# Optimization experiments

Hardware: AMD Instinct MI355X
Metric: run time of the kernel (lower is better)

## Reference

```python
import jax, jax.numpy as jnp
import numpy as np


def setup_inputs() -> dict:
    key = jax.random.key(0)
    ks = jax.random.split(key, 8)
    N, E = 10000, 160000
    IN, OUT, TC = 512, 512, 256
    x = jax.random.normal(ks[0], (N, IN), dtype=jnp.float32)
    t_emb = jax.random.normal(ks[1], (TC,), dtype=jnp.float32)
    edge_index = jax.random.randint(ks[2], (2, E), 0, N, dtype=jnp.int64)
    # GCNConv weight (glorot-ish scale) and bias
    W = jax.random.normal(ks[3], (IN, OUT), dtype=jnp.float32) / np.sqrt(IN)
    b = jnp.zeros((OUT,), dtype=jnp.float32)
    # time_proj Linear(TC, OUT)
    Wt = jax.random.normal(ks[4], (TC, OUT), dtype=jnp.float32) / np.sqrt(TC)
    bt = jnp.zeros((OUT,), dtype=jnp.float32)
    return {"x": x, "t_emb": t_emb, "edge_index": edge_index,
            "W": W, "b": b, "Wt": Wt, "bt": bt}


def _gcn_conv(x, edge_index, W, b):
    # PyG GCNConv: add self-loops, symmetric normalization, xW, scatter-add, +bias
    N = x.shape[0]
    loops = jnp.arange(N, dtype=edge_index.dtype)
    src = jnp.concatenate([edge_index[0], loops])  # [E+N]
    dst = jnp.concatenate([edge_index[1], loops])
    deg = jax.ops.segment_sum(jnp.ones_like(dst, dtype=x.dtype), dst,
                              num_segments=N)  # in-degree incl. self-loop
    dinv = jnp.where(deg > 0, jax.lax.rsqrt(deg), 0.0)
    norm = dinv[src] * dinv[dst]  # [E+N]
    xw = x @ W  # [N, OUT] - transform before gather (fewer FLOPs on edges)
    msgs = norm[:, None] * xw[src]  # [E+N, OUT]
    out = jax.ops.segment_sum(msgs, dst, num_segments=N)
    return out + b


def reference(x, t_emb, edge_index, W, b, Wt, bt):
    h = _gcn_conv(x, edge_index, W, b)          # [N, OUT]
    time_emb = t_emb @ Wt + bt                   # [OUT] (1-D t_emb branch)
    return h + time_emb
```

## Files before the change

### kernel.cpp

```cpp
#include <hip/hip_runtime.h>

#define OUTC 512
#define INC 512
#define NTILE 4
#define TCOL 128
#define LDA 72
#define TPB 256
#define CAP 96

typedef __bf16 bf16x8 __attribute__((ext_vector_type(8)));
typedef float f32x4 __attribute__((ext_vector_type(4)));

static __device__ __forceinline__ unsigned short f2bf(float f) {
    unsigned u = __float_as_uint(f);
    unsigned r = u + 0x7fffu + ((u >> 16) & 1u);
    return (unsigned short)(r >> 16);
}
static __device__ __forceinline__ float bflo(unsigned r) { return __uint_as_float(r << 16); }
static __device__ __forceinline__ float bfhi(unsigned r) { return __uint_as_float(r & 0xffff0000u); }
static __device__ __forceinline__ void acc8s(float* a, uint4 v, float n) {
    a[0] += n * bflo(v.x); a[1] += n * bfhi(v.x);
    a[2] += n * bflo(v.y); a[3] += n * bfhi(v.y);
    a[4] += n * bflo(v.z); a[5] += n * bfhi(v.z);
    a[6] += n * bflo(v.w); a[7] += n * bfhi(v.w);
}

__global__ __launch_bounds__(256) void k_prep(const float* __restrict__ x,
                                              const float* __restrict__ W,
                                              const float* __restrict__ t_emb,
                                              const float* __restrict__ Wt,
                                              const float* __restrict__ bt,
                                              const float* __restrict__ b,
                                              int* __restrict__ counts,
                                              unsigned short* __restrict__ xb,
                                              unsigned short* __restrict__ wtb,
                                              float* __restrict__ temb,
                                              int ZB, int XBB,
                                              int M, int Mpad, int TC) {
    __shared__ float smem[32 * 33];
    int bid = blockIdx.x;
    if (bid < ZB) {
        int i = bid * 256 + threadIdx.x;
        if (i < M) counts[i] = 0;
    } else if (bid < ZB + XBB) {
        int idx = (bid - ZB) * 256 + threadIdx.x;
        int row = idx >> 6;
        int kg = (idx & 63) * 8;
        ushort4 h0 = make_ushort4(0, 0, 0, 0), h1 = make_ushort4(0, 0, 0, 0);
        if (row < M) {
            float4 v0 = *(const float4*)(x + (size_t)row * INC + kg);
            float4 v1 = *(const float4*)(x + (size_t)row * INC + kg + 4);
            h0 = make_ushort4(f2bf(v0.x), f2bf(v0.y), f2bf(v0.z), f2bf(v0.w));
            h1 = make_ushort4(f2bf(v1.x), f2bf(v1.y), f2bf(v1.z), f2bf(v1.w));
        }
        *(ushort4*)(xb + (size_t)row * INC + kg) = h0;
        *(ushort4*)(xb + (size_t)row * INC + kg + 4) = h1;
    } else if (bid < ZB + XBB + 256) {
        int b2 = bid - (ZB + XBB);
        int bk = (b2 & 15) * 32, bn = (b2 >> 4) * 32;
        int tx = threadIdx.x & 31, ty = threadIdx.x >> 5;
        for (int r = ty; r < 32; r += 8)
            smem[r * 33 + tx] = W[(size_t)(bk + r) * OUTC + bn + tx];
        __syncthreads();
        for (int r = ty; r < 32; r += 8)
            wtb[(size_t)(bn + r) * INC + bk + tx] = f2bf(smem[tx * 33 + r]);
    } else {
        int j = bid - (ZB + XBB + 256);
        int t = threadIdx.x;
        float p = 0.0f;
        for (int k = t; k < TC; k += 256) p += t_emb[k] * Wt[(size_t)k * OUTC + j];
        smem[t] = p;
        __syncthreads();
        for (int s = 128; s > 0; s >>= 1) {
            if (t < s) smem[t] += smem[t + s];
            __syncthreads();
        }
        if (t == 0) temb[j] = smem[0] + bt[j] + b[j];
    }
}

__global__ __launch_bounds__(256) void k_ag(const unsigned short* __restrict__ xb,
                                            const unsigned short* __restrict__ wtb,
                                            unsigned short* __restrict__ xwb,
                                            const int* __restrict__ src,
                                            const int* __restrict__ dst,
                                            int* __restrict__ counts,
                                            int* __restrict__ slots,
                                            int E, int Mpad) {
    __shared__ unsigned short la[128 * LDA];
    __shared__ unsigned short lb[128 * LDA];

    const int bid = blockIdx.x;
    const int tid = threadIdx.x;
    const int GB = (Mpad / 128) * (OUTC / 128);

    if (bid >= GB) {
        int e = (bid - GB) * 256 + tid;
        if (e < E) {
            int s = src[e];
            int d = dst[e];
            int pos = atomicAdd(&counts[d], 1);
            if (pos < CAP) slots[(size_t)d * CAP + pos] = s;
        }
        return;
    }

    const int n0 = (bid & 3) * 128;
    const int m0 = (bid >> 2) * 128;
    const int lane = tid & 63;
    const int wave = tid >> 6;
    const int wr = (wave >> 1) * 64;
    const int wc = (wave & 1) * 64;
    const int l15 = lane & 15;
    const int k8 = (lane >> 4) * 8;

    f32x4 acc[4][4];
#pragma unroll
    for (int m = 0; m < 4; ++m)
#pragma unroll
        for (int n = 0; n < 4; ++n)
            acc[m][n] = (f32x4){0.f, 0.f, 0.f, 0.f};

    for (int k0 = 0; k0 < INC; k0 += 64) {
#pragma unroll
        for (int i = 0; i < 4; ++i) {
            int f = i * 256 + tid;
            int row = f >> 3, c = f & 7;
            uint4 va = *(const uint4*)(xb + (size_t)(m0 + row) * INC + k0 + c * 8);
            *(uint4*)(&la[row * LDA + c * 8]) = va;
            uint4 vb = *(const uint4*)(wtb + (size_t)(n0 + row) * INC + k0 + c * 8);
            *(uint4*)(&lb[row * LDA + c * 8]) = vb;
        }
        __syncthreads();

#pragma unroll
        for (int kc = 0; kc < 64; kc += 32) {
            bf16x8 af[4], bf[4];
#pragma unroll
            for (int m = 0; m < 4; ++m)
                af[m] = *(const bf16x8*)(&la[(wr + m * 16 + l15) * LDA + kc + k8]);
#pragma unroll
            for (int n = 0; n < 4; ++n)
                bf[n] = *(const bf16x8*)(&lb[(wc + n * 16 + l15) * LDA + kc + k8]);
#pragma unroll
            for (int m = 0; m < 4; ++m)
#pragma unroll
                for (int n = 0; n < 4; ++n)
                    acc[m][n] = __builtin_amdgcn_mfma_f32_16x16x32_bf16(af[m], bf[n], acc[m][n], 0, 0, 0);
        }
        __syncthreads();
    }

    const int rbase = (lane >> 4) * 4;
#pragma unroll
    for (int m = 0; m < 4; ++m)
#pragma unroll
        for (int n = 0; n < 4; ++n) {
            int gcol = n0 + wc + n * 16 + l15;
            unsigned short* p = xwb + (size_t)(gcol >> 7) * Mpad * TCOL + (gcol & 127);
#pragma unroll
            for (int r = 0; r < 4; ++r) {
                int grow = m0 + wr + m * 16 + rbase + r;
                p[(size_t)grow * TCOL] = f2bf(acc[m][n][r]);
            }
        }
}

__global__ __launch_bounds__(256) void k_gather(const int* __restrict__ slots,
                                                const int* __restrict__ counts,
                                                const unsigned short* __restrict__ xwb,
                                                const float* __restrict__ temb,
                                                float* __restrict__ out, int N, int Mpad) {
    const int bid = blockIdx.x;
    const int tile = (bid & 7) >> 1;
    const int node = (bid >> 3) * 8 + (bid & 1) * 4 + (threadIdx.x >> 6);
    if (node >= N) return;
    const int lane = threadIdx.x & 63;
    const int slot = lane >> 4;
    const int c8 = (lane & 15) * 8;
    const unsigned short* basep = xwb + (size_t)tile * Mpad * TCOL + c8;

    float a[8] = {0.f, 0.f, 0.f, 0.f, 0.f, 0.f, 0.f, 0.f};
    const int deg = counts[node];
    const int dc = deg < CAP ? deg : CAP;
    const int* sp = slots + (size_t)node * CAP;
    int i = 0;
    for (; i + 8 <= dc; i += 8) {
        int sA = sp[i + slot];
        int sB = sp[i + 4 + slot];
        uint4 vA = *(const uint4*)(basep + (size_t)sA * TCOL);
        uint4 vB = *(const uint4*)(basep + (size_t)sB * TCOL);
        float nA = rsqrtf((float)counts[sA] + 1.0f);
        float nB = rsqrtf((float)counts[sB] + 1.0f);
        acc8s(a, vA, nA);
        acc8s(a, vB, nB);
    }
    for (; i < dc; i += 4) {
        int idx = i + slot;
        int sA = node;
        float nA = 0.f;
        if (idx < dc) {
            sA = sp[idx];
            nA = rsqrtf((float)counts[sA] + 1.0f);
        }
        uint4 v = *(const uint4*)(basep + (size_t)sA * TCOL);
        acc8s(a, v, nA);
    }
#pragma unroll
    for (int k = 0; k < 8; ++k) {
        a[k] += __shfl_xor(a[k], 16, 64);
        a[k] += __shfl_xor(a[k], 32, 64);
    }
    const float di = rsqrtf((float)deg + 1.0f);
    {
        uint4 v = *(const uint4*)(basep + (size_t)node * TCOL);
        acc8s(a, v, di);
    }
    if (slot < 2) {
        const int gc = tile * TCOL + c8 + slot * 4;
        float4 tv = *(const float4*)(temb + gc);
        float4 o;
        o.x = di * a[slot * 4 + 0] + tv.x;
        o.y = di * a[slot * 4 + 1] + tv.y;
        o.z = di * a[slot * 4 + 2] + tv.z;
        o.w = di * a[slot * 4 + 3] + tv.w;
        *(float4*)(out + (size_t)node * OUTC + gc) = o;
    }
}

extern "C" void kernel_launch(void* const* d_in, const int* in_sizes, int n_in,
                              void* d_out, int out_size, void* d_ws, size_t ws_size,
                              hipStream_t stream) {
    const float* x     = (const float*)d_in[0];
    const float* t_emb = (const float*)d_in[1];
    const int*   ei    = (const int*)d_in[2];
    const float* W     = (const float*)d_in[3];
    const float* b     = (const float*)d_in[4];
    const float* Wt    = (const float*)d_in[5];
    const float* bt    = (const float*)d_in[6];
    float* out = (float*)d_out;

    const int N  = in_sizes[0] / INC;
    const int E  = in_sizes[2] / 2;
    const int TC = in_sizes[1];
    const int Mpad = (N + 127) & ~127;

    char* ws = (char*)d_ws;
    size_t off = 0;
    unsigned short* xb  = (unsigned short*)(ws + off); off += (size_t)Mpad * INC * 2;
    unsigned short* xwb = (unsigned short*)(ws + off); off += (size_t)Mpad * OUTC * 2;
    unsigned short* wtb = (unsigned short*)(ws + off); off += (size_t)INC * OUTC * 2;
    int* counts = (int*)(ws + off);        off += ((size_t)N * 4 + 255) & ~(size_t)255;
    int* slots  = (int*)(ws + off);        off += ((size_t)N * CAP * 4 + 255) & ~(size_t)255;
    float* temb = (float*)(ws + off);      off += OUTC * 4;

    const int* srcIdx = ei;
    const int* dstIdx = ei + E;

    const int ZB  = (N + 255) / 256;
    const int XBB = Mpad * (INC / 8) / 256;
    const int GB  = (Mpad / 128) * (OUTC / 128);
    const int SB  = (E + 255) / 256;

    k_prep<<<ZB + XBB + 256 + OUTC, TPB, 0, stream>>>(x, W, t_emb, Wt, bt, b,
                                                      counts, xb, wtb, temb,
                                                      ZB, XBB, N, Mpad, TC);
    k_ag<<<GB + SB, TPB, 0, stream>>>(xb, wtb, xwb, srcIdx, dstIdx,
                                      counts, slots, E, Mpad);

    const int gather_blocks = ((N + 7) / 8) * 8;
    k_gather<<<gather_blocks, TPB, 0, stream>>>(slots, counts, xwb,
                                                temb, out, N, Mpad);
}
```

Measured before the change: 127.9 us.

## Double-buffer GEMM tiles with direct global-to-LDS loads and XOR swizzle

Replaces the register-staged global→LDS copy in the bf16 MFMA GEMM with global_load_lds direct loads into a double-buffered LDS tile, prefetching the next K-slice while computing the current one. The padded LDS layout is replaced by an XOR swizzle to avoid bank conflicts without padding. This aims to hide global load latency and cut VGPR traffic, at the cost of doubling LDS use, which may lower occupancy.

```diff
diff --git a/kernel.cpp b/kernel.cpp
--- a/kernel.cpp
+++ b/kernel.cpp
@@ -4,12 +4,17 @@
 #define INC 512
 #define NTILE 4
 #define TCOL 128
-#define LDA 72
 #define TPB 256
 #define CAP 96
 
 typedef __bf16 bf16x8 __attribute__((ext_vector_type(8)));
 typedef float f32x4 __attribute__((ext_vector_type(4)));
+
+typedef __attribute__((address_space(1))) const unsigned char as1_u8;
+typedef __attribute__((address_space(3))) unsigned char as3_u8;
+static __device__ __forceinline__ void gload16(const void* g, void* l) {
+    __builtin_amdgcn_global_load_lds((as1_u8*)g, (as3_u8*)l, 16, 0, 0);
+}
 
 static __device__ __forceinline__ unsigned short f2bf(float f) {
     unsigned u = __float_as_uint(f);
@@ -87,8 +92,8 @@
                                             int* __restrict__ counts,
                                             int* __restrict__ slots,
                                             int E, int Mpad) {
-    __shared__ unsigned short la[128 * LDA];
-    __shared__ unsigned short lb[128 * LDA];
+    __shared__ unsigned short lsA[2][128 * 64];
+    __shared__ unsigned short lsB[2][128 * 64];
 
     const int bid = blockIdx.x;
     const int tid = threadIdx.x;
@@ -112,7 +117,20 @@
     const int wr = (wave >> 1) * 64;
     const int wc = (wave & 1) * 64;
     const int l15 = lane & 15;
-    const int k8 = (lane >> 4) * 8;
+    const int qb = lane >> 4;
+
+    const int l8r = lane >> 3;
+    const int swb = ((lane & 7) ^ l8r) << 4;
+
+    const unsigned char* gA[4];
+    const unsigned char* gB[4];
+#pragma unroll
+    for (int i = 0; i < 4; ++i) {
+        int c = wave * 4 + i;
+        int row = c * 8 + l8r;
+        gA[i] = (const unsigned char*)(xb + (size_t)(m0 + row) * INC) + swb;
+        gB[i] = (const unsigned char*)(wtb + (size_t)(n0 + row) * INC) + swb;
+    }
 
     f32x4 acc[4][4];
 #pragma unroll
@@ -121,35 +139,56 @@
         for (int n = 0; n < 4; ++n)
             acc[m][n] = (f32x4){0.f, 0.f, 0.f, 0.f};
 
-    for (int k0 = 0; k0 < INC; k0 += 64) {
-#pragma unroll
-        for (int i = 0; i < 4; ++i) {
-            int f = i * 256 + tid;
-            int row = f >> 3, c = f & 7;
-            uint4 va = *(const uint4*)(xb + (size_t)(m0 + row) * INC + k0 + c * 8);
-            *(uint4*)(&la[row * LDA + c * 8]) = va;
-            uint4 vb = *(const uint4*)(wtb + (size_t)(n0 + row) * INC + k0 + c * 8);
-            *(uint4*)(&lb[row * LDA + c * 8]) = vb;
-        }
+    unsigned short* pa = &lsA[0][0];
+    unsigned short* pb = &lsB[0][0];
+    unsigned short* qa = &lsA[1][0];
+    unsigned short* qbf = &lsB[1][0];
+
+#define STAGE(dA, dB, kb)                                                    \
+    {                                                                        \
+        _Pragma("unroll")                                                    \
+        for (int i = 0; i < 4; ++i) {                                        \
+            int c = wave * 4 + i;                                            \
+            gload16(gA[i] + (kb) * 2, (unsigned char*)(dA) + c * 1024);      \
+            gload16(gB[i] + (kb) * 2, (unsigned char*)(dB) + c * 1024);      \
+        }                                                                    \
+    }
+
+    STAGE(pa, pb, 0);
+    __syncthreads();
+
+    for (int t = 0; t < INC / 64; ++t) {
+        if (t < INC / 64 - 1) STAGE(qa, qbf, (t + 1) * 64);
+
+#pragma unroll
+        for (int kc = 0; kc < 64; kc += 32) {
+            const int q = (kc >> 3) + qb;
+            bf16x8 af[4], bv[4];
+#pragma unroll
+            for (int m = 0; m < 4; ++m) {
+                int row = wr + m * 16 + l15;
+                af[m] = *(const bf16x8*)((const unsigned char*)pa + row * 128 +
+                                         ((q ^ (row & 7)) << 4));
+            }
+#pragma unroll
+            for (int n = 0; n < 4; ++n) {
+                int row = wc + n * 16 + l15;
+                bv[n] = *(const bf16x8*)((const unsigned char*)pb + row * 128 +
+                                         ((q ^ (row & 7)) << 4));
+            }
+#pragma unroll
+            for (int m = 0; m < 4; ++m)
+#pragma unroll
+                for (int n = 0; n < 4; ++n)
+                    acc[m][n] = __builtin_amdgcn_mfma_f32_16x16x32_bf16(af[m], bv[n], acc[m][n], 0, 0, 0);
+        }
+
         __syncthreads();
-
-#pragma unroll
-        for (int kc = 0; kc < 64; kc += 32) {
-            bf16x8 af[4], bf[4];
-#pragma unroll
-            for (int m = 0; m < 4; ++m)
-                af[m] = *(const bf16x8*)(&la[(wr + m * 16 + l15) * LDA + kc + k8]);
-#pragma unroll
-            for (int n = 0; n < 4; ++n)
-                bf[n] = *(const bf16x8*)(&lb[(wc + n * 16 + l15) * LDA + kc + k8]);
-#pragma unroll
-            for (int m = 0; m < 4; ++m)
-#pragma unroll
-                for (int n = 0; n < 4; ++n)
-                    acc[m][n] = __builtin_amdgcn_mfma_f32_16x16x32_bf16(af[m], bf[n], acc[m][n], 0, 0, 0);
-        }
-        __syncthreads();
-    }
+        unsigned short* tmp;
+        tmp = pa; pa = qa; qa = tmp;
+        tmp = pb; pb = qbf; qbf = tmp;
+    }
+#undef STAGE
 
     const int rbase = (lane >> 4) * 4;
 #pragma unroll
```

After: 127.0 us. Within noise of the previous version (-0.8%).
